# Optimization experiments

Measured on AMD Instinct MI355X. Metric: run time of the kernel, lower is better.

Reference implementation:

```python
import jax, jax.numpy as jnp
import numpy as np

B, T, H, HEADS, OUT = 16, 8192, 256, 2, 5
PERIOD = 16  # phoneme boundary every 16 frames
EPS_DENOM = 1e-5
LN_EPS = 1e-5
TEMP = 1.0


def setup_inputs() -> dict:
    key = jax.random.key(0)
    ks = jax.random.split(key, 8)
    s = 0.02
    feat = jax.random.normal(ks[0], (B, T, H), jnp.float32)
    ph_bd = jnp.broadcast_to(((jnp.arange(T) % PERIOD) == PERIOD - 1).astype(jnp.int32), (B, T))
    ph_length = T // PERIOD + 1  # 513
    return {
        'feat': feat,
        'ph_bd': ph_bd,
        'ph_length': ph_length,
        'w_attn': jax.random.normal(ks[1], (HEADS, H), jnp.float32) * s,
        'b_attn': jnp.zeros((HEADS,), jnp.float32),
        'ln1_g': jnp.ones((H,), jnp.float32),
        'ln1_b': jnp.zeros((H,), jnp.float32),
        'conv1_w': jax.random.normal(ks[2], (H, H, 3), jnp.float32) * s,
        'conv1_b': jnp.zeros((H,), jnp.float32),
        'conv2_w': jax.random.normal(ks[3], (H, H, 1), jnp.float32) * s,
        'conv2_b': jnp.zeros((H,), jnp.float32),
        'ln2_g': jnp.ones((H,), jnp.float32),
        'ln2_b': jnp.zeros((H,), jnp.float32),
        'post_w': jax.random.normal(ks[4], (H, H, 3), jnp.float32) * s,
        'post_b': jnp.zeros((H,), jnp.float32),
        'w_out': jax.random.normal(ks[5], (OUT, H), jnp.float32) * s,
        'b_out': jnp.zeros((OUT,), jnp.float32),
    }


def _ln_c(x, g, b):
    # LayerNorm over channel dim of [B, C, L]
    m = jnp.mean(x, axis=1, keepdims=True)
    v = jnp.mean((x - m) ** 2, axis=1, keepdims=True)
    return (x - m) * jax.lax.rsqrt(v + LN_EPS) * g[None, :, None] + b[None, :, None]


def _conv1d(x, w, b):
    # x: [B, C, L], w: [O, I, K], 'same' padding
    pad = (w.shape[-1] - 1) // 2
    y = jax.lax.conv_general_dilated(x, w, (1,), [(pad, pad)],
                                     dimension_numbers=('NCH', 'OIH', 'NCH'))
    return y + b[None, :, None]


def reference(feat, ph_bd, ph_length, w_attn, b_attn, ln1_g, ln1_b,
              conv1_w, conv1_b, conv2_w, conv2_b, ln2_g, ln2_b,
              post_w, post_b, w_out, b_out):
    # multihead attention weights per frame: [B, T, heads]
    attn = jax.nn.sigmoid(jnp.einsum('bth,ah->bta', feat, w_attn) + b_attn)
    attn_mean = jnp.mean(attn, axis=-1)                 # [B, T]
    # mean over heads of feat[...,None]*attn == feat * mean(attn)
    attn_feat = feat * attn_mean[..., None]             # [B, T, H]

    mel2ph = jnp.cumsum(ph_bd, axis=1)                  # [B, T] frame->phoneme id
    bidx = jnp.arange(feat.shape[0])[:, None]
    denom = jnp.zeros((feat.shape[0], ph_length), feat.dtype).at[bidx, mel2ph].add(attn_mean)
    ph_agg = jnp.zeros((feat.shape[0], ph_length, feat.shape[2]), feat.dtype).at[bidx, mel2ph].add(attn_feat)
    ph_agg = ph_agg / (denom[..., None] + EPS_DENOM)    # [B, L, H]

    # ConvBlocks (1 residual block, layers_in_block=1, c_multiple=1, swish)
    x = jnp.transpose(ph_agg, (0, 2, 1))                # [B, H, L]
    nonpad = (jnp.sum(jnp.abs(x), axis=1) > 0).astype(x.dtype)[:, None, :]
    h = _ln_c(x, ln1_g, ln1_b)
    h = _conv1d(h, conv1_w, conv1_b) * (3.0 ** -0.5)
    h = jax.nn.silu(h)
    h = _conv1d(h, conv2_w, conv2_b)
    x = (x + h) * nonpad
    x = _ln_c(x, ln2_g, ln2_b) * nonpad
    x = _conv1d(x, post_w, post_b) * nonpad
    out = jnp.transpose(x, (0, 2, 1))                   # [B, L, H]

    tech_logits = (jnp.einsum('blh,oh->blo', out, w_out) + b_out) / TEMP
    return tech_logits
```

## Files before the change

### kernel.cpp

```cpp
#include <hip/hip_runtime.h>
#include <hip/hip_bf16.h>

#define TDIM 8192
#define BDIM 16
#define HDIM 256
#define PHL  513
#define PADL 515
#define MROWS (BDIM*PHL)
#define SEGW 514

typedef __attribute__((ext_vector_type(8))) short  short8;
typedef __attribute__((ext_vector_type(4))) float  floatx4;

__device__ __forceinline__ float sigmoidf_(float x){ return 1.0f/(1.0f+__expf(-x)); }

typedef __attribute__((address_space(1))) const unsigned int gu32;
typedef __attribute__((address_space(3))) unsigned int lu32;
__device__ __forceinline__ void g2l16(const void* g, void* l){
  __builtin_amdgcn_global_load_lds((gu32*)g, (lu32*)l, 16, 0, 0);
}

__device__ __forceinline__ float blk_reduce(float v, float* red){
  #pragma unroll
  for (int off=32; off>0; off>>=1) v += __shfl_xor(v, off, 64);
  int w = threadIdx.x>>6;
  __syncthreads();
  if ((threadIdx.x&63)==0) red[w]=v;
  __syncthreads();
  return red[0]+red[1]+red[2]+red[3];
}

__global__ __launch_bounds__(256) void k_init(
    const int* __restrict__ ph_bd, int* __restrict__ seg,
    const float* __restrict__ conv1_w, const float* __restrict__ conv2_w,
    const float* __restrict__ post_w,
    __bf16* __restrict__ w1t, __bf16* __restrict__ w2t, __bf16* __restrict__ w3t,
    int* __restrict__ rowoff,
    float* __restrict__ x0pad, __bf16* __restrict__ h1pad, __bf16* __restrict__ x2pad)
{
  int tid = threadIdx.x;
  if (blockIdx.x < BDIM){
    int b = blockIdx.x;
    const int* in = ph_bd + (size_t)b*TDIM;
    int sb = b*SEGW;
    int base = tid*32;
    int vals[32]; int s=0;
    #pragma unroll
    for (int i=0;i<32;i+=4){
      int4 v = *(const int4*)(in+base+i);
      vals[i]=v.x; vals[i+1]=v.y; vals[i+2]=v.z; vals[i+3]=v.w;
      s += v.x+v.y+v.z+v.w;
    }
    __shared__ int ls[256];
    ls[tid]=s; __syncthreads();
    for (int off=1; off<256; off<<=1){
      int t = (tid>=off)? ls[tid-off] : 0;
      __syncthreads();
      ls[tid]+=t;
      __syncthreads();
    }
    int cur = ls[tid]-s;
    #pragma unroll
    for (int i=0;i<32;i++){
      int nxt = cur + vals[i];
      for (int v=cur+1; v<=nxt; v++) seg[sb+v] = base+i;
      cur = nxt;
    }
    if (tid==0) seg[sb] = 0;
    if (tid==255){ for (int v=cur+1; v<SEGW; v++) seg[sb+v] = TDIM; }
    return;
  }
  int idx = (blockIdx.x-BDIM)*256 + tid;
  if (idx < 256*768){
    int o = idx/768, j = idx - o*768;
    int dl = j>>8, i = j&255;
    int src = (o*256+i)*3 + dl;
    w1t[idx] = (__bf16)conv1_w[src];
    w3t[idx] = (__bf16)post_w[src];
  }
  if (idx < 256*256)
    w2t[idx] = (__bf16)conv2_w[idx];
  if (idx < MROWS){
    int b = idx/513, l = idx - b*513;
    rowoff[idx] = (b*PADL + l)*HDIM;
  }
  if (idx < BDIM*2*HDIM){
    int b = idx>>9, rr=(idx>>8)&1, c=idx&255;
    size_t row = (size_t)b*PADL + (rr? (PADL-1):0);
    x0pad[row*HDIM+c]=0.f;
    h1pad[row*HDIM+c]=(__bf16)0.f;
    x2pad[row*HDIM+c]=(__bf16)0.f;
  }
}

__global__ __launch_bounds__(256) void k_attn(
    const float* __restrict__ feat, const int* __restrict__ seg,
    const float* __restrict__ w_attn, const float* __restrict__ b_attn,
    const float* __restrict__ ln1_g, const float* __restrict__ ln1_b,
    float* __restrict__ x0pad, __bf16* __restrict__ h1pad, float* __restrict__ nonpad)
{
  int b = blockIdx.x / PHL, p = blockIdx.x - b*PHL;
  int tid = threadIdx.x, lane = tid&63, w = tid>>6;
  __shared__ float4 sfeat[16*64];
  __shared__ float sam[16];
  __shared__ float red[4];

  int t0 = seg[b*SEGW + p], t1 = seg[b*SEGW + p + 1];

  float4 wa0 = ((const float4*)w_attn)[lane];
  float4 wa1 = ((const float4*)(w_attn+HDIM))[lane];
  float ba0 = b_attn[0], ba1 = b_attn[1];

  float agg=0.f, denom=0.f;
  for (int base=t0; base<t1; base+=16){
    int nf = min(16, t1-base);
    const float4* src = (const float4*)(feat + ((size_t)b*TDIM + base)*HDIM);
    for (int idx=tid; idx<nf*64; idx+=256) sfeat[idx] = src[idx];
    __syncthreads();
    for (int ft=w; ft<nf; ft+=4){
      float4 f = sfeat[ft*64+lane];
      float d0 = f.x*wa0.x + f.y*wa0.y + f.z*wa0.z + f.w*wa0.w;
      float d1 = f.x*wa1.x + f.y*wa1.y + f.z*wa1.z + f.w*wa1.w;
      #pragma unroll
      for (int off=32;off>0;off>>=1){ d0+=__shfl_xor(d0,off,64); d1+=__shfl_xor(d1,off,64); }
      if (lane==0) sam[ft] = 0.5f*(sigmoidf_(d0+ba0)+sigmoidf_(d1+ba1));
    }
    __syncthreads();
    const float* sf = (const float*)sfeat;
    for (int ft=0; ft<nf; ft++){ float a=sam[ft]; agg += sf[ft*HDIM+tid]*a; denom += a; }
    __syncthreads();
  }

  float x = agg/(denom+1e-5f);
  float sabs = blk_reduce(fabsf(x), red);
  float np = (sabs>0.f)?1.f:0.f;
  float mean = blk_reduce(x, red)*(1.f/HDIM);
  float d = x-mean;
  float var = blk_reduce(d*d, red)*(1.f/HDIM);
  float h = d*rsqrtf(var+1e-5f)*ln1_g[tid]+ln1_b[tid];

  size_t off = ((size_t)b*PADL + p + 1)*HDIM;
  x0pad[off+tid]=x;
  h1pad[off+tid]=(__bf16)h;
  if (tid==0) nonpad[blockIdx.x]=np;
}

__global__ __launch_bounds__(256) void k_convblock(
    const short* __restrict__ h1pad, const int* __restrict__ rowoff,
    const short* __restrict__ w1t, const short* __restrict__ w2t,
    const float* __restrict__ c1b, const float* __restrict__ c2b,
    const float* __restrict__ x0pad, const float* __restrict__ nonpad,
    const float* __restrict__ g2, const float* __restrict__ b2,
    __bf16* __restrict__ x2pad)
{
  __shared__ __align__(16) short As[4*32*8];
  __shared__ __align__(16) short Bs[4*256*8];
  __shared__ __align__(16) short Gt[32*32*8];
  __shared__ float s_sum[4][16], s_ssq[4][16];
  int tid=threadIdx.x, lane=tid&63, w=tid>>6, quad=lane>>4, l15=lane&15;
  int g = w>>1, n0w = (w&1)*128;
  int m0 = blockIdx.x*32;
  int arow = min(m0 + (lane&31), MROWS-1);
  const short* aPtr = h1pad + rowoff[arow] + (2*w + (lane>>5))*8;

  floatx4 acc[8];
  #pragma unroll
  for (int i=0;i<8;i++) acc[i] = (floatx4){0.f,0.f,0.f,0.f};

  for (int chunk=0; chunk<24; chunk++){
    int k0 = chunk*32;
    if (w < 2) g2l16(aPtr + k0, &As[w*64*8]);
    #pragma unroll
    for (int ng=0; ng<4; ng++)
      g2l16(w1t + (size_t)(ng*64+lane)*768 + k0 + w*8, &Bs[(w*256 + ng*64)*8]);
    __syncthreads();
    short8 af = *(const short8*)&As[(quad*32 + g*16 + l15)*8];
    #pragma unroll
    for (int nt=0; nt<8; nt++){
      short8 bf = *(const short8*)&Bs[(quad*256 + n0w + nt*16 + l15)*8];
      acc[nt] = __builtin_amdgcn_mfma_f32_16x16x32_bf16(af, bf, acc[nt], 0,0,0);
    }
    __syncthreads();
  }

  const float inv_s3 = 0.57735026918962576f;
  #pragma unroll
  for (int nt=0; nt<8; nt++){
    int n = n0w + nt*16 + l15;
    float bias = c1b[n];
    #pragma unroll
    for (int r=0;r<4;r++){
      float v = (acc[nt][r] + bias)*inv_s3;
      v = v*sigmoidf_(v);
      int m = g*16 + quad*4 + r;
      ((__bf16*)Gt)[((n>>3)*32 + m)*8 + (n&7)] = (__bf16)v;
    }
  }

  floatx4 acc2[8];
  #pragma unroll
  for (int i=0;i<8;i++) acc2[i] = (floatx4){0.f,0.f,0.f,0.f};
  for (int chunk=0; chunk<8; chunk++){
    int k0 = chunk*32;
    #pragma unroll
    for (int ng=0; ng<4; ng++)
      g2l16(w2t + (size_t)(ng*64+lane)*256 + k0 + w*8, &Bs[(w*256 + ng*64)*8]);
    __syncthreads();
    short8 af = *(const short8*)&Gt[((chunk*4+quad)*32 + g*16 + l15)*8];
    #pragma unroll
    for (int nt=0; nt<8; nt++){
      short8 bf = *(const short8*)&Bs[(quad*256 + n0w + nt*16 + l15)*8];
      acc2[nt] = __builtin_amdgcn_mfma_f32_16x16x32_bf16(af, bf, acc2[nt], 0,0,0);
    }
    __syncthreads();
  }

  int mbase = m0 + g*16 + quad*4;
  float np_[4]; int roff[4];
  #pragma unroll
  for (int r=0;r<4;r++){
    int mm = min(mbase + r, MROWS-1);
    np_[r] = nonpad[mm];
    roff[r] = rowoff[mm] + HDIM;
  }
  float sum[4]={0,0,0,0}, ssq[4]={0,0,0,0};
  #pragma unroll
  for (int nt=0; nt<8; nt++){
    int n = n0w + nt*16 + l15;
    float cb = c2b[n];
    #pragma unroll
    for (int r=0;r<4;r++){
      float x = (x0pad[roff[r]+n] + acc2[nt][r] + cb)*np_[r];
      acc2[nt][r] = x;
      sum[r]+=x; ssq[r]+=x*x;
    }
  }
  #pragma unroll
  for (int off=1; off<16; off<<=1){
    #pragma unroll
    for (int r=0;r<4;r++){ sum[r]+=__shfl_xor(sum[r],off,64); ssq[r]+=__shfl_xor(ssq[r],off,64); }
  }
  if (l15==0){
    #pragma unroll
    for (int r=0;r<4;r++){ s_sum[w][quad*4+r]=sum[r]; s_ssq[w][quad*4+r]=ssq[r]; }
  }
  __syncthreads();
  float mean[4], rs[4];
  #pragma unroll
  for (int r=0;r<4;r++){
    int i = quad*4+r;
    float ts = s_sum[w&~1][i] + s_sum[w|1][i];
    float tq = s_ssq[w&~1][i] + s_ssq[w|1][i];
    mean[r] = ts*(1.f/HDIM);
    float var = tq*(1.f/HDIM) - mean[r]*mean[r];
    rs[r] = rsqrtf(var+1e-5f);
  }
  #pragma unroll
  for (int nt=0; nt<8; nt++){
    int n = n0w + nt*16 + l15;
    float gg=g2[n], bb=b2[n];
    #pragma unroll
    for (int r=0;r<4;r++){
      if (mbase + r < MROWS){
        float y = ((acc2[nt][r]-mean[r])*rs[r]*gg + bb)*np_[r];
        x2pad[roff[r]+n] = (__bf16)y;
      }
    }
  }
}

__global__ __launch_bounds__(256) void k_post(
    const short* __restrict__ x2pad, const int* __restrict__ rowoff,
    const short* __restrict__ w3t, const float* __restrict__ postb,
    const float* __restrict__ nonpad, const float* __restrict__ w_out,
    const float* __restrict__ b_out, float* __restrict__ dst)
{
  __shared__ __align__(16) short As[4*32*8];
  __shared__ __align__(16) short Bs[4*256*8];
  __shared__ float ws[5*256];
  __shared__ float s_log[4][16][5];
  int tid=threadIdx.x, lane=tid&63, w=tid>>6, quad=lane>>4, l15=lane&15;
  int g = w>>1, n0w = (w&1)*128;
  int m0 = blockIdx.x*32;
  int arow = min(m0 + (lane&31), MROWS-1);
  const short* aPtr = x2pad + rowoff[arow] + (2*w + (lane>>5))*8;
  for (int i=tid; i<5*256; i+=256) ws[i]=w_out[i];

  floatx4 acc[8];
  #pragma unroll
  for (int i=0;i<8;i++) acc[i] = (floatx4){0.f,0.f,0.f,0.f};
  for (int chunk=0; chunk<24; chunk++){
    int k0 = chunk*32;
    if (w < 2) g2l16(aPtr + k0, &As[w*64*8]);
    #pragma unroll
    for (int ng=0; ng<4; ng++)
      g2l16(w3t + (size_t)(ng*64+lane)*768 + k0 + w*8, &Bs[(w*256 + ng*64)*8]);
    __syncthreads();
    short8 af = *(const short8*)&As[(quad*32 + g*16 + l15)*8];
    #pragma unroll
    for (int nt=0; nt<8; nt++){
      short8 bf = *(const short8*)&Bs[(quad*256 + n0w + nt*16 + l15)*8];
      acc[nt] = __builtin_amdgcn_mfma_f32_16x16x32_bf16(af, bf, acc[nt], 0,0,0);
    }
    __syncthreads();
  }

  int mbase = m0 + g*16 + quad*4;
  float np_[4];
  #pragma unroll
  for (int r=0;r<4;r++) np_[r] = nonpad[min(mbase+r, MROWS-1)];
  float p[4][5];
  #pragma unroll
  for (int r=0;r<4;r++)
    #pragma unroll
    for (int o=0;o<5;o++) p[r][o]=0.f;
  #pragma unroll
  for (int nt=0; nt<8; nt++){
    int n = n0w + nt*16 + l15;
    float pb = postb[n];
    float wv[5];
    #pragma unroll
    for (int o=0;o<5;o++) wv[o]=ws[o*256+n];
    #pragma unroll
    for (int r=0;r<4;r++){
      float v = (acc[nt][r] + pb)*np_[r];
      #pragma unroll
      for (int o=0;o<5;o++) p[r][o] += v*wv[o];
    }
  }
  #pragma unroll
  for (int off=1; off<16; off<<=1)
    #pragma unroll
    for (int r=0;r<4;r++)
      #pragma unroll
      for (int o=0;o<5;o++) p[r][o]+=__shfl_xor(p[r][o],off,64);
  if (l15==0){
    #pragma unroll
    for (int r=0;r<4;r++)
      #pragma unroll
      for (int o=0;o<5;o++) s_log[w][quad*4+r][o]=p[r][o];
  }
  __syncthreads();
  if (l15==0 && (w&1)==0){
    #pragma unroll
    for (int r=0;r<4;r++){
      int m = mbase + r;
      if (m < MROWS){
        int i = quad*4+r;
        #pragma unroll
        for (int o=0;o<5;o++)
          dst[(size_t)m*5+o] = s_log[w][i][o] + s_log[w+1][i][o] + b_out[o];
      }
    }
  }
}

extern "C" void kernel_launch(void* const* d_in, const int* in_sizes, int n_in,
                              void* d_out, int out_size, void* d_ws, size_t ws_size,
                              hipStream_t stream) {
  const float* feat    = (const float*)d_in[0];
  const int*   ph_bd   = (const int*)  d_in[1];
  const float* w_attn  = (const float*)d_in[3];
  const float* b_attn  = (const float*)d_in[4];
  const float* ln1_g   = (const float*)d_in[5];
  const float* ln1_b   = (const float*)d_in[6];
  const float* conv1_w = (const float*)d_in[7];
  const float* conv1_b = (const float*)d_in[8];
  const float* conv2_w = (const float*)d_in[9];
  const float* conv2_b = (const float*)d_in[10];
  const float* ln2_g   = (const float*)d_in[11];
  const float* ln2_b   = (const float*)d_in[12];
  const float* post_w  = (const float*)d_in[13];
  const float* post_b  = (const float*)d_in[14];
  const float* w_out   = (const float*)d_in[15];
  const float* b_out   = (const float*)d_in[16];

  char* wp = (char*)d_ws;
  auto alloc = [&](size_t bytes)->void*{
    void* p = (void*)wp; wp += (bytes + 255) & ~(size_t)255; return p;
  };
  int*    seg    = (int*)   alloc((size_t)BDIM*SEGW*4);
  int*    rowoff = (int*)   alloc((size_t)MROWS*4);
  float*  x0pad  = (float*) alloc((size_t)BDIM*PADL*HDIM*4);
  __bf16* h1pad  = (__bf16*)alloc((size_t)BDIM*PADL*HDIM*2);
  __bf16* x2pad  = (__bf16*)alloc((size_t)BDIM*PADL*HDIM*2);
  float*  nonpad = (float*) alloc((size_t)MROWS*4);
  __bf16* w1t    = (__bf16*)alloc((size_t)256*768*2);
  __bf16* w2t    = (__bf16*)alloc((size_t)256*256*2);
  __bf16* w3t    = (__bf16*)alloc((size_t)256*768*2);

  k_init<<<BDIM+768, 256, 0, stream>>>(ph_bd, seg, conv1_w, conv2_w, post_w,
                                       w1t, w2t, w3t, rowoff, x0pad, h1pad, x2pad);
  k_attn<<<MROWS, 256, 0, stream>>>(feat, seg, w_attn, b_attn,
                                    ln1_g, ln1_b, x0pad, h1pad, nonpad);
  k_convblock<<<257, 256, 0, stream>>>((const short*)h1pad, rowoff, (const short*)w1t,
                                       (const short*)w2t, conv1_b, conv2_b,
                                       x0pad, nonpad, ln2_g, ln2_b, x2pad);
  k_post<<<257, 256, 0, stream>>>((const short*)x2pad, rowoff, (const short*)w3t,
                                  post_b, nonpad, w_out, b_out, (float*)d_out);
}
```

Baseline: 301.8 us.

## Halve conv GEMM row tile and stage input halo rows once in LDS

The conv-block and post-conv GEMM kernels now use 16-row tiles instead of 32, which doubles the block count to 513 so more CUs have work. Each block copies its 16 rows plus the halo rows of the padded activation into LDS once. The three conv taps then read shifted rows from that buffer instead of streaming A through global-to-LDS loads on every chunk. The cost is that each block reloads the full weight matrices, so weight traffic is doubled, and the rows that span a batch boundary need extra index remapping.

```diff
diff --git a/kernel.cpp b/kernel.cpp
--- a/kernel.cpp
+++ b/kernel.cpp
@@ -153,31 +153,38 @@
     const float* __restrict__ g2, const float* __restrict__ b2,
     __bf16* __restrict__ x2pad)
 {
-  __shared__ __align__(16) short As[4*32*8];
+  __shared__ __align__(16) short As[20*264];
   __shared__ __align__(16) short Bs[4*256*8];
-  __shared__ __align__(16) short Gt[32*32*8];
+  __shared__ __align__(16) short Gt[32*16*8];
   __shared__ float s_sum[4][16], s_ssq[4][16];
   int tid=threadIdx.x, lane=tid&63, w=tid>>6, quad=lane>>4, l15=lane&15;
-  int g = w>>1, n0w = (w&1)*128;
-  int m0 = blockIdx.x*32;
-  int arow = min(m0 + (lane&31), MROWS-1);
-  const short* aPtr = h1pad + rowoff[arow] + (2*w + (lane>>5))*8;
-
-  floatx4 acc[8];
-  #pragma unroll
-  for (int i=0;i<8;i++) acc[i] = (floatx4){0.f,0.f,0.f,0.f};
-
-  for (int chunk=0; chunk<24; chunk++){
-    int k0 = chunk*32;
-    if (w < 2) g2l16(aPtr + k0, &As[w*64*8]);
+  int m0 = blockIdx.x*16;
+  int batch = m0/513, l0 = m0 - batch*513;
+  int s = min(16, 513-l0);
+  int ro0 = rowoff[m0];
+  int ro1 = rowoff[min(m0+s, MROWS-1)];
+  for (int t=tid; t<20*32; t+=256){
+    int j=t>>5, c8=t&31;
+    int src = (j<=s+1)? ro0 + j*256 : ro1 + (j-s-2)*256;
+    *(short8*)&As[j*264 + c8*8] = *(const short8*)&h1pad[src + c8*8];
+  }
+  int radj = l15 + (l15>=s ? 2:0);
+
+  floatx4 acc[4];
+  #pragma unroll
+  for (int i=0;i<4;i++) acc[i] = (floatx4){0.f,0.f,0.f,0.f};
+
+  for (int c=0; c<24; c++){
+    int k0 = c*32;
     #pragma unroll
     for (int ng=0; ng<4; ng++)
       g2l16(w1t + (size_t)(ng*64+lane)*768 + k0 + w*8, &Bs[(w*256 + ng*64)*8]);
     __syncthreads();
-    short8 af = *(const short8*)&As[(quad*32 + g*16 + l15)*8];
-    #pragma unroll
-    for (int nt=0; nt<8; nt++){
-      short8 bf = *(const short8*)&Bs[(quad*256 + n0w + nt*16 + l15)*8];
+    int dl = c>>3, kk = (c&7)*32 + quad*8;
+    short8 af = *(const short8*)&As[(radj+dl)*264 + kk];
+    #pragma unroll
+    for (int nt=0; nt<4; nt++){
+      short8 bf = *(const short8*)&Bs[(quad*256 + w*64 + nt*16 + l15)*8];
       acc[nt] = __builtin_amdgcn_mfma_f32_16x16x32_bf16(af, bf, acc[nt], 0,0,0);
     }
     __syncthreads();
@@ -185,48 +192,47 @@
 
   const float inv_s3 = 0.57735026918962576f;
   #pragma unroll
-  for (int nt=0; nt<8; nt++){
-    int n = n0w + nt*16 + l15;
+  for (int nt=0; nt<4; nt++){
+    int n = w*64 + nt*16 + l15;
     float bias = c1b[n];
     #pragma unroll
     for (int r=0;r<4;r++){
       float v = (acc[nt][r] + bias)*inv_s3;
       v = v*sigmoidf_(v);
-      int m = g*16 + quad*4 + r;
-      ((__bf16*)Gt)[((n>>3)*32 + m)*8 + (n&7)] = (__bf16)v;
-    }
-  }
-
-  floatx4 acc2[8];
-  #pragma unroll
-  for (int i=0;i<8;i++) acc2[i] = (floatx4){0.f,0.f,0.f,0.f};
-  for (int chunk=0; chunk<8; chunk++){
-    int k0 = chunk*32;
+      int m = quad*4 + r;
+      ((__bf16*)Gt)[((n>>3)*16 + m)*8 + (n&7)] = (__bf16)v;
+    }
+  }
+
+  floatx4 acc2[4];
+  #pragma unroll
+  for (int i=0;i<4;i++) acc2[i] = (floatx4){0.f,0.f,0.f,0.f};
+  for (int c=0; c<8; c++){
+    int k0 = c*32;
     #pragma unroll
     for (int ng=0; ng<4; ng++)
       g2l16(w2t + (size_t)(ng*64+lane)*256 + k0 + w*8, &Bs[(w*256 + ng*64)*8]);
     __syncthreads();
-    short8 af = *(const short8*)&Gt[((chunk*4+quad)*32 + g*16 + l15)*8];
-    #pragma unroll
-    for (int nt=0; nt<8; nt++){
-      short8 bf = *(const short8*)&Bs[(quad*256 + n0w + nt*16 + l15)*8];
+    short8 af = *(const short8*)&Gt[((c*4+quad)*16 + l15)*8];
+    #pragma unroll
+    for (int nt=0; nt<4; nt++){
+      short8 bf = *(const short8*)&Bs[(quad*256 + w*64 + nt*16 + l15)*8];
       acc2[nt] = __builtin_amdgcn_mfma_f32_16x16x32_bf16(af, bf, acc2[nt], 0,0,0);
     }
     __syncthreads();
   }
 
-  int mbase = m0 + g*16 + quad*4;
   float np_[4]; int roff[4];
   #pragma unroll
   for (int r=0;r<4;r++){
-    int mm = min(mbase + r, MROWS-1);
-    np_[r] = nonpad[mm];
-    roff[r] = rowoff[mm] + HDIM;
+    int m = m0 + quad*4 + r;
+    np_[r] = nonpad[m];
+    roff[r] = rowoff[m] + HDIM;
   }
   float sum[4]={0,0,0,0}, ssq[4]={0,0,0,0};
   #pragma unroll
-  for (int nt=0; nt<8; nt++){
-    int n = n0w + nt*16 + l15;
+  for (int nt=0; nt<4; nt++){
+    int n = w*64 + nt*16 + l15;
     float cb = c2b[n];
     #pragma unroll
     for (int r=0;r<4;r++){
@@ -249,22 +255,20 @@
   #pragma unroll
   for (int r=0;r<4;r++){
     int i = quad*4+r;
-    float ts = s_sum[w&~1][i] + s_sum[w|1][i];
-    float tq = s_ssq[w&~1][i] + s_ssq[w|1][i];
+    float ts = s_sum[0][i]+s_sum[1][i]+s_sum[2][i]+s_sum[3][i];
+    float tq = s_ssq[0][i]+s_ssq[1][i]+s_ssq[2][i]+s_ssq[3][i];
     mean[r] = ts*(1.f/HDIM);
     float var = tq*(1.f/HDIM) - mean[r]*mean[r];
     rs[r] = rsqrtf(var+1e-5f);
   }
   #pragma unroll
-  for (int nt=0; nt<8; nt++){
-    int n = n0w + nt*16 + l15;
+  for (int nt=0; nt<4; nt++){
+    int n = w*64 + nt*16 + l15;
     float gg=g2[n], bb=b2[n];
     #pragma unroll
     for (int r=0;r<4;r++){
-      if (mbase + r < MROWS){
-        float y = ((acc2[nt][r]-mean[r])*rs[r]*gg + bb)*np_[r];
-        x2pad[roff[r]+n] = (__bf16)y;
-      }
+      float y = ((acc2[nt][r]-mean[r])*rs[r]*gg + bb)*np_[r];
+      x2pad[roff[r]+n] = (__bf16)y;
     }
   }
 }
@@ -275,48 +279,54 @@
     const float* __restrict__ nonpad, const float* __restrict__ w_out,
     const float* __restrict__ b_out, float* __restrict__ dst)
 {
-  __shared__ __align__(16) short As[4*32*8];
+  __shared__ __align__(16) short As[20*264];
   __shared__ __align__(16) short Bs[4*256*8];
   __shared__ float ws[5*256];
   __shared__ float s_log[4][16][5];
   int tid=threadIdx.x, lane=tid&63, w=tid>>6, quad=lane>>4, l15=lane&15;
-  int g = w>>1, n0w = (w&1)*128;
-  int m0 = blockIdx.x*32;
-  int arow = min(m0 + (lane&31), MROWS-1);
-  const short* aPtr = x2pad + rowoff[arow] + (2*w + (lane>>5))*8;
+  int m0 = blockIdx.x*16;
+  int batch = m0/513, l0 = m0 - batch*513;
+  int s = min(16, 513-l0);
+  int ro0 = rowoff[m0];
+  int ro1 = rowoff[min(m0+s, MROWS-1)];
+  for (int t=tid; t<20*32; t+=256){
+    int j=t>>5, c8=t&31;
+    int src = (j<=s+1)? ro0 + j*256 : ro1 + (j-s-2)*256;
+    *(short8*)&As[j*264 + c8*8] = *(const short8*)&x2pad[src + c8*8];
+  }
   for (int i=tid; i<5*256; i+=256) ws[i]=w_out[i];
-
-  floatx4 acc[8];
-  #pragma unroll
-  for (int i=0;i<8;i++) acc[i] = (floatx4){0.f,0.f,0.f,0.f};
-  for (int chunk=0; chunk<24; chunk++){
-    int k0 = chunk*32;
-    if (w < 2) g2l16(aPtr + k0, &As[w*64*8]);
+  int radj = l15 + (l15>=s ? 2:0);
+
+  floatx4 acc[4];
+  #pragma unroll
+  for (int i=0;i<4;i++) acc[i] = (floatx4){0.f,0.f,0.f,0.f};
+  for (int c=0; c<24; c++){
+    int k0 = c*32;
     #pragma unroll
     for (int ng=0; ng<4; ng++)
       g2l16(w3t + (size_t)(ng*64+lane)*768 + k0 + w*8, &Bs[(w*256 + ng*64)*8]);
     __syncthreads();
-    short8 af = *(const short8*)&As[(quad*32 + g*16 + l15)*8];
-    #pragma unroll
-    for (int nt=0; nt<8; nt++){
-      short8 bf = *(const short8*)&Bs[(quad*256 + n0w + nt*16 + l15)*8];
+    int dl = c>>3, kk = (c&7)*32 + quad*8;
+    short8 af = *(const short8*)&As[(radj+dl)*264 + kk];
+    #pragma unroll
+    for (int nt=0; nt<4; nt++){
+      short8 bf = *(const short8*)&Bs[(quad*256 + w*64 + nt*16 + l15)*8];
       acc[nt] = __builtin_amdgcn_mfma_f32_16x16x32_bf16(af, bf, acc[nt], 0,0,0);
     }
     __syncthreads();
   }
 
-  int mbase = m0 + g*16 + quad*4;
   float np_[4];
   #pragma unroll
-  for (int r=0;r<4;r++) np_[r] = nonpad[min(mbase+r, MROWS-1)];
+  for (int r=0;r<4;r++) np_[r] = nonpad[m0 + quad*4 + r];
   float p[4][5];
   #pragma unroll
   for (int r=0;r<4;r++)
     #pragma unroll
     for (int o=0;o<5;o++) p[r][o]=0.f;
   #pragma unroll
-  for (int nt=0; nt<8; nt++){
-    int n = n0w + nt*16 + l15;
+  for (int nt=0; nt<4; nt++){
+    int n = w*64 + nt*16 + l15;
     float pb = postb[n];
     float wv[5];
     #pragma unroll
@@ -341,17 +351,10 @@
       for (int o=0;o<5;o++) s_log[w][quad*4+r][o]=p[r][o];
   }
   __syncthreads();
-  if (l15==0 && (w&1)==0){
-    #pragma unroll
-    for (int r=0;r<4;r++){
-      int m = mbase + r;
-      if (m < MROWS){
-        int i = quad*4+r;
-        #pragma unroll
-        for (int o=0;o<5;o++)
-          dst[(size_t)m*5+o] = s_log[w][i][o] + s_log[w+1][i][o] + b_out[o];
-      }
-    }
+  if (tid < 80){
+    int row = tid/5, o = tid - row*5;
+    float v = s_log[0][row][o]+s_log[1][row][o]+s_log[2][row][o]+s_log[3][row][o];
+    dst[(size_t)(m0+row)*5 + o] = v + b_out[o];
   }
 }
 
@@ -393,9 +396,9 @@
                                        w1t, w2t, w3t, rowoff, x0pad, h1pad, x2pad);
   k_attn<<<MROWS, 256, 0, stream>>>(feat, seg, w_attn, b_attn,
                                     ln1_g, ln1_b, x0pad, h1pad, nonpad);
-  k_convblock<<<257, 256, 0, stream>>>((const short*)h1pad, rowoff, (const short*)w1t,
+  k_convblock<<<513, 256, 0, stream>>>((const short*)h1pad, rowoff, (const short*)w1t,
                                        (const short*)w2t, conv1_b, conv2_b,
                                        x0pad, nonpad, ln2_g, ln2_b, x2pad);
-  k_post<<<257, 256, 0, stream>>>((const short*)x2pad, rowoff, (const short*)w3t,
+  k_post<<<513, 256, 0, stream>>>((const short*)x2pad, rowoff, (const short*)w3t,
                                   post_b, nonpad, w_out, b_out, (float*)d_out);
 }
```

Result: slower. 318.7 us (+5.6%).
